# Kernel tuning notes

Hardware: AMD Instinct MI355X
Metric: run time of the kernel (lower is better)

Reference implementation:

```python
import jax, jax.numpy as jnp
import numpy as np

N_NODES = 50000
N_EDGES = 600000
IN_F, HID_F, OUT_F = 128, 128, 64


def setup_inputs() -> dict:
    key = jax.random.key(0)
    ks = jax.random.split(key, 7)
    features = jax.random.normal(ks[0], (N_NODES, IN_F), jnp.float32)
    W1 = jax.random.normal(ks[1], (IN_F, HID_F), jnp.float32) / np.sqrt(IN_F)
    b1 = jnp.zeros((HID_F,), jnp.float32)
    W2 = jax.random.normal(ks[2], (HID_F, OUT_F), jnp.float32) / np.sqrt(HID_F)
    b2 = jnp.zeros((OUT_F,), jnp.float32)
    edge_src = jax.random.randint(ks[3], (N_EDGES,), 0, N_NODES, jnp.int32)
    edge_dst = jax.random.randint(ks[4], (N_EDGES,), 0, N_NODES, jnp.int32)
    return {"features": features, "W1": W1, "b1": b1, "W2": W2, "b2": b2,
            "edge_src": edge_src, "edge_dst": edge_dst}


def _graph_conv(h, W, b, edge_src, edge_dst, norm_src, norm_dst, n_nodes):
    # DGL GraphConv, norm='both': D_in^{-1/2} A D_out^{-1/2} (h W) + b
    # Apply W first (linear commutes with the linear aggregation) to minimize
    # the size of the gathered edge tensor when out <= in.
    h = (h * norm_src[:, None]) @ W                       # [N, d_out]
    agg = jax.ops.segment_sum(h[edge_src], edge_dst, num_segments=n_nodes)
    return agg * norm_dst[:, None] + b


def reference(features, W1, b1, W2, b2, edge_src, edge_dst):
    n_nodes = features.shape[0]
    ones = jnp.ones(edge_src.shape[0], features.dtype)
    out_deg = jax.ops.segment_sum(ones, edge_src, num_segments=n_nodes)
    in_deg = jax.ops.segment_sum(ones, edge_dst, num_segments=n_nodes)
    norm_src = jnp.clip(out_deg, 1.0) ** -0.5             # source-side D_out^{-1/2}
    norm_dst = jnp.clip(in_deg, 1.0) ** -0.5              # dest-side   D_in^{-1/2}
    h = _graph_conv(features, W1, b1, edge_src, edge_dst, norm_src, norm_dst, n_nodes)
    h = jax.nn.relu(h)
    h = _graph_conv(h, W2, b2, edge_src, edge_dst, norm_src, norm_dst, n_nodes)
    return h
```

## Files before the change

kernel.cpp:

```cpp
#include <hip/hip_runtime.h>


typedef unsigned short u16;
typedef unsigned int u32;
typedef short s16x8 __attribute__((ext_vector_type(8)));
typedef float f32x4 __attribute__((ext_vector_type(4)));
typedef u32 u32x4 __attribute__((ext_vector_type(4)));

__device__ __forceinline__ float bf2f(u16 u) {
    return __uint_as_float((u32)u << 16);
}
__device__ __forceinline__ u16 f2bf(float f) {
    u32 u = __float_as_uint(f);
    u += 0x7fff + ((u >> 16) & 1);
    return (u16)(u >> 16);
}


__global__ __launch_bounds__(256) void hist_part(const int* __restrict__ src,
                                                 const int* __restrict__ dst,
                                                 u32* __restrict__ part) {
    __shared__ u32 cnt[6250];
    const int s = blockIdx.x;
    const int r = blockIdx.y;
    const int z = blockIdx.z;
    const int lo = r * 12500;
    for (int t = threadIdx.x; t < 6250; t += 256) cnt[t] = 0;
    __syncthreads();
    const int* ids = z ? dst : src;
    const int base = s * 37500;
    for (int e0 = base; e0 < base + 37500; e0 += 1024) {
        int idx[4];
#pragma unroll
        for (int k = 0; k < 4; ++k) {
            int e = e0 + k * 256 + threadIdx.x;
            idx[k] = (e < base + 37500) ? ids[e] : -1;
        }
#pragma unroll
        for (int k = 0; k < 4; ++k) {
            unsigned local = (unsigned)(idx[k] - lo);
            if (local < 12500u)
                atomicAdd(&cnt[local >> 1], 1u << ((local & 1) * 16));
        }
    }
    __syncthreads();
    u32* out = part + (size_t)(z * 16 + s) * 25000 + r * 6250;
    for (int t = threadIdx.x; t < 6250; t += 256) out[t] = cnt[t];
}

__global__ __launch_bounds__(256) void reduce_norm_sniff(const u32* __restrict__ part,
                                                         int* __restrict__ degd,
                                                         float* __restrict__ ns,
                                                         float* __restrict__ nd,
                                                         int* __restrict__ bsum,
                                                         const u16* __restrict__ X16,
                                                         int* __restrict__ flag) {
    __shared__ int sh[256];
    if (blockIdx.x == 0) {
        u16 v = X16[threadIdx.x * 2];
        int e = (v >> 7) & 0xFF;
        sh[threadIdx.x] = (e >= 0x30 && e <= 0x47) ? 1 : 0;
        __syncthreads();
        for (int off = 128; off > 0; off >>= 1) {
            if (threadIdx.x < off) sh[threadIdx.x] += sh[threadIdx.x + off];
            __syncthreads();
        }
        if (threadIdx.x == 0) *flag = (sh[0] >= 128) ? 1 : 0;
        __syncthreads();
    }
    int i = blockIdx.x * 256 + threadIdx.x;
    u32 a = 0, b = 0;
    if (i < 50000) {
        const int w = i >> 1, h = (i & 1) * 16;
#pragma unroll
        for (int s = 0; s < 16; ++s) {
            a += (part[(size_t)s * 25000 + w] >> h) & 0xffffu;
            b += (part[(size_t)(16 + s) * 25000 + w] >> h) & 0xffffu;
        }
        degd[i] = (int)b;
        ns[i] = rsqrtf((float)(a > 1 ? a : 1));
        nd[i] = rsqrtf((float)(b > 1 ? b : 1));
    }
    sh[threadIdx.x] = (i < 50000) ? (int)b : 0;
    __syncthreads();
    for (int off = 128; off > 0; off >>= 1) {
        if (threadIdx.x < off) sh[threadIdx.x] += sh[threadIdx.x + off];
        __syncthreads();
    }
    if (threadIdx.x == 0) bsum[blockIdx.x] = sh[0];
}

__global__ __launch_bounds__(256) void rowptr_scan(const int* __restrict__ degd,
                                                   const int* __restrict__ bsum,
                                                   int* __restrict__ rp,
                                                   int* __restrict__ cur,
                                                   int n, int nb) {
    __shared__ int sb[256];
    __shared__ int sh[256];
    const int t = threadIdx.x;
    sb[t] = (t < nb && t < (int)blockIdx.x) ? bsum[t] : 0;
    int i = blockIdx.x * 256 + t;
    int v = (i < n) ? degd[i] : 0;
    sh[t] = v;
    __syncthreads();
    for (int off = 128; off > 0; off >>= 1) {
        if (t < off) sb[t] += sb[t + off];
        __syncthreads();
    }
    const int boff = sb[0];
    for (int off = 1; off < 256; off <<= 1) {
        int x = (t >= off) ? sh[t - off] : 0;
        __syncthreads();
        sh[t] += x;
        __syncthreads();
    }
    if (i < n) {
        int e = boff + sh[t] - v;
        rp[i] = e;
        cur[i] = e;
        if (i == n - 1) rp[n] = e + v;
    }
}

template <int FO, bool X_ALWAYS_BF16>
__device__ __forceinline__ void gemm_body(u32* __restrict__ Xs,
                                          const void* __restrict__ Xv,
                                          const void* __restrict__ Wv,
                                          int flag,
                                          const float* __restrict__ ns,
                                          u16* __restrict__ Ylo,
                                          u16* __restrict__ Yhi,
                                          int split, int nrows, int bx) {
    constexpr int NCT = FO / 64;
    const int tid = threadIdx.x;
    const int nb = bx * 64;

    const bool xbf = X_ALWAYS_BF16 ? true : (flag != 0);
    if (xbf) {
        const u32* Xg = (const u32*)Xv;
        for (int t = tid; t < 64 * 64; t += 256) {
            int row = t >> 6, cp = t & 63;
            int r = nb + row;
            Xs[row * 68 + cp] = (r < nrows) ? Xg[(size_t)r * 64 + cp] : 0u;
        }
    } else {
        const float* Xg = (const float*)Xv;
        for (int t = tid; t < 64 * 64; t += 256) {
            int row = t >> 6, cp = t & 63;
            int r = nb + row;
            u32 lo = 0, hi = 0;
            if (r < nrows) {
                lo = f2bf(Xg[(size_t)r * 128 + 2 * cp]);
                hi = f2bf(Xg[(size_t)r * 128 + 2 * cp + 1]);
            }
            Xs[row * 68 + cp] = lo | (hi << 16);
        }
    }

    const int lane = tid & 63;
    const int wv = tid >> 6;
    const int lr = lane & 15;
    const int g = lane >> 4;
    const int cbase = wv * (FO / 4);

    u32 bf[NCT][4][4];
    if (flag) {
        const u32* Wg = (const u32*)Wv;
#pragma unroll
        for (int c = 0; c < NCT; ++c) {
            const int col = cbase + c * 16 + lr;
            const int ce = col >> 1, sh = (col & 1) * 16;
#pragma unroll
            for (int t = 0; t < 4; ++t)
#pragma unroll
                for (int p = 0; p < 4; ++p) {
                    const int kp = t * 16 + g * 4 + p;
                    u32 lo = (Wg[(size_t)(2 * kp) * (FO / 2) + ce] >> sh) & 0xffffu;
                    u32 hi = (Wg[(size_t)(2 * kp + 1) * (FO / 2) + ce] >> sh) & 0xffffu;
                    bf[c][t][p] = lo | (hi << 16);
                }
        }
    } else {
        const float* Wg = (const float*)Wv;
#pragma unroll
        for (int c = 0; c < NCT; ++c) {
            const int col = cbase + c * 16 + lr;
#pragma unroll
            for (int t = 0; t < 4; ++t)
#pragma unroll
                for (int p = 0; p < 4; ++p) {
                    const int kp = t * 16 + g * 4 + p;
                    u32 lo = f2bf(Wg[(size_t)(2 * kp) * FO + col]);
                    u32 hi = f2bf(Wg[(size_t)(2 * kp + 1) * FO + col]);
                    bf[c][t][p] = lo | (hi << 16);
                }
        }
    }
    __syncthreads();

    union U4 { u32x4 u; s16x8 s; };
#pragma unroll
    for (int rt = 0; rt < 4; ++rt) {
        U4 a[4];
#pragma unroll
        for (int t = 0; t < 4; ++t)
            a[t].u = *(const u32x4*)&Xs[(rt * 16 + lr) * 68 + t * 16 + g * 4];
        const int rq = nb + rt * 16 + g * 4;
        float nsv[4];
#pragma unroll
        for (int q = 0; q < 4; ++q) nsv[q] = ns[rq + q];
#pragma unroll
        for (int c = 0; c < NCT; ++c) {
            f32x4 acc = {0.f, 0.f, 0.f, 0.f};
#pragma unroll
            for (int t = 0; t < 4; ++t) {
                U4 b;
                b.u = (u32x4){bf[c][t][0], bf[c][t][1], bf[c][t][2], bf[c][t][3]};
                acc = __builtin_amdgcn_mfma_f32_16x16x32_bf16(a[t].s, b.s, acc,
                                                              0, 0, 0);
            }
            const int cc = cbase + c * 16 + lr;
#pragma unroll
            for (int q = 0; q < 4; ++q) {
                int r = rq + q;
                if (r < nrows) {
                    u16* Y = (r < split) ? (Ylo + (size_t)r * FO)
                                         : (Yhi + (size_t)(r - split) * FO);
                    Y[cc] = f2bf(acc[q] * nsv[q]);
                }
            }
        }
    }
}

__global__ __launch_bounds__(256) void gemm1_fill(
        const void* __restrict__ Xv, const void* __restrict__ Wv,
        const int* __restrict__ flagp, const float* __restrict__ ns,
        u16* __restrict__ Ylo, u16* __restrict__ Yhi, int split, int nrows,
        const int* __restrict__ esrc, const int* __restrict__ edst,
        int* __restrict__ cur, int* __restrict__ col, int nedges, int fillb) {
    __shared__ __align__(16) u32 Xs[64 * 68];
    if ((int)blockIdx.x < fillb) {
        int i = blockIdx.x * 256 + threadIdx.x;
        if (i < nedges) {
            int pos = atomicAdd(&cur[edst[i]], 1);
            col[pos] = esrc[i];
        }
        return;
    }
    gemm_body<128, false>(Xs, Xv, Wv, *flagp, ns, Ylo, Yhi, split, nrows,
                          (int)blockIdx.x - fillb);
}

template <int FO, bool X_ALWAYS_BF16>
__global__ __launch_bounds__(256) void gemm_mfma(const void* __restrict__ Xv,
                                                 const void* __restrict__ Wv,
                                                 const int* __restrict__ flagp,
                                                 const float* __restrict__ ns,
                                                 u16* __restrict__ Ylo,
                                                 u16* __restrict__ Yhi,
                                                 int split, int nrows) {
    __shared__ __align__(16) u32 Xs[64 * 68];
    gemm_body<FO, X_ALWAYS_BF16>(Xs, Xv, Wv, *flagp, ns, Ylo, Yhi, split,
                                 nrows, (int)blockIdx.x);
}

__device__ __forceinline__ const u32* h128row(const u16* Hlo, const u16* Hhi,
                                              int split, int s) {
    return (const u32*)((s < split) ? (Hlo + (size_t)s * 128)
                                    : (Hhi + (size_t)(s - split) * 128));
}
__device__ __forceinline__ void g128_drain(const u16* __restrict__ Hlo,
                                           const u16* __restrict__ Hhi, int split,
                                           const int* __restrict__ col,
                                           int e, int pend, int lane,
                                           float& a0, float& a1) {
    for (; e + 8 <= pend; e += 8) {
        u32 u[8];
#pragma unroll
        for (int t = 0; t < 8; ++t)
            u[t] = h128row(Hlo, Hhi, split, col[e + t])[lane];
#pragma unroll
        for (int t = 0; t < 8; ++t) {
            a0 += bf2f((u16)(u[t] & 0xffff));
            a1 += bf2f((u16)(u[t] >> 16));
        }
    }
    for (; e + 4 <= pend; e += 4) {
        u32 u[4];
#pragma unroll
        for (int t = 0; t < 4; ++t)
            u[t] = h128row(Hlo, Hhi, split, col[e + t])[lane];
#pragma unroll
        for (int t = 0; t < 4; ++t) {
            a0 += bf2f((u16)(u[t] & 0xffff));
            a1 += bf2f((u16)(u[t] >> 16));
        }
    }
    for (; e < pend; ++e) {
        u32 u = h128row(Hlo, Hhi, split, col[e])[lane];
        a0 += bf2f((u16)(u & 0xffff));
        a1 += bf2f((u16)(u >> 16));
    }
}

__global__ __launch_bounds__(256) void gather128(const u16* __restrict__ Hlo,
                                                 const u16* __restrict__ Hhi, int split,
                                                 const int* __restrict__ rp,
                                                 const int* __restrict__ col,
                                                 const float* __restrict__ nd,
                                                 const void* __restrict__ bias,
                                                 const int* __restrict__ flagp,
                                                 u16* __restrict__ out, int nnodes) {
    int wv = threadIdx.x >> 6, lane = threadIdx.x & 63;
    int n0 = blockIdx.x * 8 + wv * 2;
    if (n0 >= nnodes) return;
    int n1 = n0 + 1;
    int pa = rp[n0], pae = rp[n0 + 1];
    int pb = rp[n1], pbe = rp[n1 + 1];
    float a0 = 0.f, a1 = 0.f, b0 = 0.f, b1 = 0.f;
    while (pa + 8 <= pae && pb + 8 <= pbe) {
        int sa[8], sb[8];
#pragma unroll
        for (int t = 0; t < 8; ++t) sa[t] = col[pa + t];
#pragma unroll
        for (int t = 0; t < 8; ++t) sb[t] = col[pb + t];
        u32 ua[8], ub[8];
#pragma unroll
        for (int t = 0; t < 8; ++t) ua[t] = h128row(Hlo, Hhi, split, sa[t])[lane];
#pragma unroll
        for (int t = 0; t < 8; ++t) ub[t] = h128row(Hlo, Hhi, split, sb[t])[lane];
#pragma unroll
        for (int t = 0; t < 8; ++t) {
            a0 += bf2f((u16)(ua[t] & 0xffff));
            a1 += bf2f((u16)(ua[t] >> 16));
            b0 += bf2f((u16)(ub[t] & 0xffff));
            b1 += bf2f((u16)(ub[t] >> 16));
        }
        pa += 8;
        pb += 8;
    }
    g128_drain(Hlo, Hhi, split, col, pa, pae, lane, a0, a1);
    g128_drain(Hlo, Hhi, split, col, pb, pbe, lane, b0, b1);
    int flag = *flagp;
    float bb0 = flag ? bf2f(((const u16*)bias)[lane * 2]) : ((const float*)bias)[lane * 2];
    float bb1 = flag ? bf2f(((const u16*)bias)[lane * 2 + 1]) : ((const float*)bias)[lane * 2 + 1];
    float va = nd[n0], vb = nd[n1];
    u32 pa32 = (u32)f2bf(fmaxf(a0 * va + bb0, 0.f))
             | ((u32)f2bf(fmaxf(a1 * va + bb1, 0.f)) << 16);
    u32 pb32 = (u32)f2bf(fmaxf(b0 * vb + bb0, 0.f))
             | ((u32)f2bf(fmaxf(b1 * vb + bb1, 0.f)) << 16);
    ((u32*)(out + (size_t)n0 * 128))[lane] = pa32;
    ((u32*)(out + (size_t)n1 * 128))[lane] = pb32;
}

__device__ __forceinline__ void g64_drain(const u16* __restrict__ H,
                                          const int* __restrict__ col,
                                          int e, int pend, int lane, float& a) {
    for (; e + 8 <= pend; e += 8) {
        float f[8];
#pragma unroll
        for (int t = 0; t < 8; ++t)
            f[t] = bf2f(H[(size_t)col[e + t] * 64 + lane]);
#pragma unroll
        for (int t = 0; t < 8; ++t) a += f[t];
    }
    for (; e + 4 <= pend; e += 4) {
        float f[4];
#pragma unroll
        for (int t = 0; t < 4; ++t)
            f[t] = bf2f(H[(size_t)col[e + t] * 64 + lane]);
#pragma unroll
        for (int t = 0; t < 4; ++t) a += f[t];
    }
    for (; e < pend; ++e)
        a += bf2f(H[(size_t)col[e] * 64 + lane]);
}

__global__ __launch_bounds__(256) void gather64(const u16* __restrict__ H,
                                                const int* __restrict__ rp,
                                                const int* __restrict__ col,
                                                const float* __restrict__ nd,
                                                const void* __restrict__ bias,
                                                const int* __restrict__ flagp,
                                                void* __restrict__ outv, int nnodes) {
    int wv = threadIdx.x >> 6, lane = threadIdx.x & 63;
    int n0 = blockIdx.x * 8 + wv * 2;
    if (n0 >= nnodes) return;
    int n1 = n0 + 1;
    int pa = rp[n0], pae = rp[n0 + 1];
    int pb = rp[n1], pbe = rp[n1 + 1];
    float a = 0.f, b = 0.f;
    while (pa + 8 <= pae && pb + 8 <= pbe) {
        float fa[8], fb[8];
#pragma unroll
        for (int t = 0; t < 8; ++t)
            fa[t] = bf2f(H[(size_t)col[pa + t] * 64 + lane]);
#pragma unroll
        for (int t = 0; t < 8; ++t)
            fb[t] = bf2f(H[(size_t)col[pb + t] * 64 + lane]);
#pragma unroll
        for (int t = 0; t < 8; ++t) { a += fa[t]; b += fb[t]; }
        pa += 8;
        pb += 8;
    }
    g64_drain(H, col, pa, pae, lane, a);
    g64_drain(H, col, pb, pbe, lane, b);
    int flag = *flagp;
    float bb = flag ? bf2f(((const u16*)bias)[lane]) : ((const float*)bias)[lane];
    float oa = a * nd[n0] + bb;
    float ob = b * nd[n1] + bb;
    if (flag) {
        ((u16*)outv)[(size_t)n0 * 64 + lane] = f2bf(oa);
        ((u16*)outv)[(size_t)n1 * 64 + lane] = f2bf(ob);
    } else {
        ((float*)outv)[(size_t)n0 * 64 + lane] = oa;
        ((float*)outv)[(size_t)n1 * 64 + lane] = ob;
    }
}

extern "C" void kernel_launch(void* const* d_in, const int* in_sizes, int n_in,
                              void* d_out, int out_size, void* d_ws, size_t ws_size,
                              hipStream_t stream) {
    constexpr int N = 50000;
    constexpr int E = 600000;
    constexpr int NB = (N + 255) / 256;
    constexpr int SPLIT = 25000;
    constexpr int FB = (E + 255) / 256;
    constexpr int GB = (N + 63) / 64;

    const void* X  = d_in[0];
    const void* W1 = d_in[1];
    const void* b1 = d_in[2];
    const void* W2 = d_in[3];
    const void* b2 = d_in[4];
    const int* esrc = (const int*)d_in[5];
    const int* edst = (const int*)d_in[6];

    char* p = (char*)d_ws;
    auto take = [&](size_t bytes) -> char* {
        char* r = p;
        p += (bytes + 255) & ~(size_t)255;
        return r;
    };
    int* flagp  = (int*)take(256);
    int* deg_d  = (int*)take((size_t)N * 4);
    float* ns   = (float*)take((size_t)N * 4);
    float* nd   = (float*)take((size_t)N * 4);
    int* bsum   = (int*)take((size_t)NB * 4);
    int* rp     = (int*)take((size_t)(N + 1) * 4);
    int* cur    = (int*)take((size_t)N * 4);
    int* col    = (int*)take((size_t)E * 4);
    u16* h0hi   = (u16*)take((size_t)(N - SPLIT) * 128 * 2);
    u16* a2     = (u16*)take((size_t)N * 128 * 2);
    size_t NEED = (size_t)(p - (char*)d_ws);

    if (ws_size < NEED) {
        hipMemsetAsync(d_out, 0, (size_t)out_size * 2, stream);
        return;
    }

    u16* h0lo = (u16*)d_out;

    u32* part = (u32*)a2;

    hist_part<<<dim3(16, 4, 2), 256, 0, stream>>>(esrc, edst, part);
    reduce_norm_sniff<<<NB, 256, 0, stream>>>(part, deg_d, ns, nd, bsum,
                                              (const u16*)X, flagp);
    rowptr_scan<<<NB, 256, 0, stream>>>(deg_d, bsum, rp, cur, N, NB);

    gemm1_fill<<<FB + GB, 256, 0, stream>>>(X, W1, flagp, ns, h0lo, h0hi,
                                            SPLIT, N, esrc, edst, cur, col,
                                            E, FB);

    gather128<<<(N + 7) / 8, 256, 0, stream>>>(h0lo, h0hi, SPLIT, rp, col, nd,
                                               b1, flagp, a2, N);

    u16* h1b = h0hi;
    gemm_mfma<64, true><<<(N + 63) / 64, 256, 0, stream>>>(
        a2, W2, flagp, ns, h1b, h1b, N, N);
    gather64<<<(N + 7) / 8, 256, 0, stream>>>(h1b, rp, col, nd, b2, flagp,
                                              d_out, N);

    (void)in_sizes; (void)n_in; (void)out_size;
}
```

Measured before the change: 222.7 us.

## Fill CSR columns via LDS cursors seeded from per-slice histogram prefix

The CSR fill no longer uses global atomics on a cursor array. Each of 128 blocks owns one edge slice and one destination range, and seeds cursors in LDS from the row pointers plus the per-slice partial counts of earlier slices. It then scatters with shared-memory atomics. The histogram kernel is re-tiled to 8 ranges so that its partial counts line up with the fill blocks, and the cur array and its initialisation in the scan are removed. The cost is fewer, heavier fill blocks that each rescan their whole slice and read 15 partial counts per node.

```diff
diff --git a/kernel.cpp b/kernel.cpp
--- a/kernel.cpp
+++ b/kernel.cpp
@@ -20,12 +20,12 @@
 __global__ __launch_bounds__(256) void hist_part(const int* __restrict__ src,
                                                  const int* __restrict__ dst,
                                                  u32* __restrict__ part) {
-    __shared__ u32 cnt[6250];
+    __shared__ u32 cnt[3125];
     const int s = blockIdx.x;
     const int r = blockIdx.y;
     const int z = blockIdx.z;
-    const int lo = r * 12500;
-    for (int t = threadIdx.x; t < 6250; t += 256) cnt[t] = 0;
+    const int lo = r * 6250;
+    for (int t = threadIdx.x; t < 3125; t += 256) cnt[t] = 0;
     __syncthreads();
     const int* ids = z ? dst : src;
     const int base = s * 37500;
@@ -39,13 +39,13 @@
 #pragma unroll
         for (int k = 0; k < 4; ++k) {
             unsigned local = (unsigned)(idx[k] - lo);
-            if (local < 12500u)
+            if (local < 6250u)
                 atomicAdd(&cnt[local >> 1], 1u << ((local & 1) * 16));
         }
     }
     __syncthreads();
-    u32* out = part + (size_t)(z * 16 + s) * 25000 + r * 6250;
-    for (int t = threadIdx.x; t < 6250; t += 256) out[t] = cnt[t];
+    u32* out = part + (size_t)(z * 16 + s) * 25000 + r * 3125;
+    for (int t = threadIdx.x; t < 3125; t += 256) out[t] = cnt[t];
 }
 
 __global__ __launch_bounds__(256) void reduce_norm_sniff(const u32* __restrict__ part,
@@ -93,7 +93,6 @@
 __global__ __launch_bounds__(256) void rowptr_scan(const int* __restrict__ degd,
                                                    const int* __restrict__ bsum,
                                                    int* __restrict__ rp,
-                                                   int* __restrict__ cur,
                                                    int n, int nb) {
     __shared__ int sb[256];
     __shared__ int sh[256];
@@ -117,7 +116,6 @@
     if (i < n) {
         int e = boff + sh[t] - v;
         rp[i] = e;
-        cur[i] = e;
         if (i == n - 1) rp[n] = e + v;
     }
 }
@@ -238,17 +236,46 @@
         const int* __restrict__ flagp, const float* __restrict__ ns,
         u16* __restrict__ Ylo, u16* __restrict__ Yhi, int split, int nrows,
         const int* __restrict__ esrc, const int* __restrict__ edst,
-        int* __restrict__ cur, int* __restrict__ col, int nedges, int fillb) {
-    __shared__ __align__(16) u32 Xs[64 * 68];
+        const int* __restrict__ rp, const u32* __restrict__ part,
+        int* __restrict__ col, int fillb) {
+    __shared__ __align__(16) u32 shmem[6400];
     if ((int)blockIdx.x < fillb) {
-        int i = blockIdx.x * 256 + threadIdx.x;
-        if (i < nedges) {
-            int pos = atomicAdd(&cur[edst[i]], 1);
-            col[pos] = esrc[i];
+        const int s = blockIdx.x & 15;
+        const int r = blockIdx.x >> 4;
+        const int lo = r * 6250;
+        u32* cursor = shmem;
+        for (int t = threadIdx.x; t < 6250; t += 256) {
+            const int i = lo + t;
+            const int w = i >> 1, h = (i & 1) * 16;
+            u32 seed = (u32)rp[i];
+#pragma unroll
+            for (int s2 = 0; s2 < 15; ++s2) {
+                u32 v = (part[(size_t)(16 + s2) * 25000 + w] >> h) & 0xffffu;
+                seed += (s2 < s) ? v : 0u;
+            }
+            cursor[t] = seed;
+        }
+        __syncthreads();
+        const int base = s * 37500;
+        for (int e0 = base; e0 < base + 37500; e0 += 1024) {
+            int d[4], ev[4];
+#pragma unroll
+            for (int k = 0; k < 4; ++k) {
+                ev[k] = e0 + k * 256 + threadIdx.x;
+                d[k] = (ev[k] < base + 37500) ? edst[ev[k]] : -1;
+            }
+#pragma unroll
+            for (int k = 0; k < 4; ++k) {
+                unsigned local = (unsigned)(d[k] - lo);
+                if (local < 6250u) {
+                    u32 pos = atomicAdd(&cursor[local], 1u);
+                    col[pos] = esrc[ev[k]];
+                }
+            }
         }
         return;
     }
-    gemm_body<128, false>(Xs, Xv, Wv, *flagp, ns, Ylo, Yhi, split, nrows,
+    gemm_body<128, false>(shmem, Xv, Wv, *flagp, ns, Ylo, Yhi, split, nrows,
                           (int)blockIdx.x - fillb);
 }
 
@@ -426,7 +453,7 @@
     constexpr int E = 600000;
     constexpr int NB = (N + 255) / 256;
     constexpr int SPLIT = 25000;
-    constexpr int FB = (E + 255) / 256;
+    constexpr int FB = 16 * 8;
     constexpr int GB = (N + 63) / 64;
 
     const void* X  = d_in[0];
@@ -449,7 +476,6 @@
     float* nd   = (float*)take((size_t)N * 4);
     int* bsum   = (int*)take((size_t)NB * 4);
     int* rp     = (int*)take((size_t)(N + 1) * 4);
-    int* cur    = (int*)take((size_t)N * 4);
     int* col    = (int*)take((size_t)E * 4);
     u16* h0hi   = (u16*)take((size_t)(N - SPLIT) * 128 * 2);
     u16* a2     = (u16*)take((size_t)N * 128 * 2);
@@ -464,14 +490,14 @@
 
     u32* part = (u32*)a2;
 
-    hist_part<<<dim3(16, 4, 2), 256, 0, stream>>>(esrc, edst, part);
+    hist_part<<<dim3(16, 8, 2), 256, 0, stream>>>(esrc, edst, part);
     reduce_norm_sniff<<<NB, 256, 0, stream>>>(part, deg_d, ns, nd, bsum,
                                               (const u16*)X, flagp);
-    rowptr_scan<<<NB, 256, 0, stream>>>(deg_d, bsum, rp, cur, N, NB);
+    rowptr_scan<<<NB, 256, 0, stream>>>(deg_d, bsum, rp, N, NB);
 
     gemm1_fill<<<FB + GB, 256, 0, stream>>>(X, W1, flagp, ns, h0lo, h0hi,
-                                            SPLIT, N, esrc, edst, cur, col,
-                                            E, FB);
+                                            SPLIT, N, esrc, edst, rp, part,
+                                            col, FB);
 
     gather128<<<(N + 7) / 8, 256, 0, stream>>>(h0lo, h0hi, SPLIT, rp, col, nd,
                                                b1, flagp, a2, N);
```

Measured after the change: 232.6 us. +4.4%, slower.
